# Kernel optimization log

Hardware: AMD Instinct MI355X
Metric: run time of the kernel (lower is better)

Reference implementation:

```python
import jax, jax.numpy as jnp
import numpy as np

RENDER_STEP = 0.005
N_FREQS = 6

def pos_enc(x):
    # x: [N,3] -> [N, 3 + 2*N_FREQS*3]
    freqs = (2.0 ** jnp.arange(N_FREQS, dtype=x.dtype)) * jnp.pi
    xb = x[:, None, :] * freqs[:, None]            # [N,F,3]
    enc = jnp.concatenate([jnp.sin(xb), jnp.cos(xb)], axis=-1).reshape(x.shape[0], -1)
    return jnp.concatenate([x, enc], axis=-1)

def geom_fwd(points, Wg0, bg0, Wg1, bg1, Wg2, bg2):
    h = jax.nn.relu(pos_enc(points) @ Wg0 + bg0)
    h = jax.nn.relu(h @ Wg1 + bg1)
    return h @ Wg2 + bg2                           # [N,16]; ch0 = sdf, full vec = features


def setup_inputs() -> dict:
    key = jax.random.key(0)
    ks = jax.random.split(key, 12)
    n_rays, n_samples = 16384, 524288
    sc = lambda fan_in: 1.0 / np.sqrt(fan_in)
    inp = {
        'rays_o': jax.random.normal(ks[0], (n_rays, 3), jnp.float32) * 0.5,
        'rays_d': jax.random.normal(ks[1], (n_rays, 3), jnp.float32),
        'ray_indices': jnp.sort(jax.random.randint(ks[2], (n_samples,), 0, n_rays, jnp.int32)),
        't_starts': jax.random.uniform(ks[3], (n_samples, 1), jnp.float32),
        'random_points': jax.random.normal(ks[4], (1024, 3), jnp.float32),
        's_var': jnp.ones((1,), jnp.float32),
        'Wg0': jax.random.normal(ks[5], (39, 256), jnp.float32) * sc(39),
        'bg0': jnp.zeros((256,), jnp.float32),
        'Wg1': jax.random.normal(ks[6], (256, 256), jnp.float32) * sc(256),
        'bg1': jnp.zeros((256,), jnp.float32),
        'Wg2': jax.random.normal(ks[7], (256, 16), jnp.float32) * sc(256),
        'bg2': jnp.zeros((16,), jnp.float32),
        'Wc0': jax.random.normal(ks[8], (25, 256), jnp.float32) * sc(25),
        'bc0': jnp.zeros((256,), jnp.float32),
        'Wc1': jax.random.normal(ks[9], (256, 3), jnp.float32) * sc(256),
        'bc1': jnp.zeros((3,), jnp.float32),
    }
    return inp


def reference(rays_o, rays_d, ray_indices, t_starts, random_points, s_var,
              Wg0, bg0, Wg1, bg1, Wg2, bg2, Wc0, bc0, Wc1, bc1):
    n_rays = rays_o.shape[0]
    rays_d = rays_d / (jnp.linalg.norm(rays_d, axis=-1, keepdims=True) + 1e-10)

    midpoints = t_starts + RENDER_STEP * 0.5       # [N,1]
    t_intervals = RENDER_STEP
    t_origins = rays_o[ray_indices]                # gather [N,3]
    t_dirs = rays_d[ray_indices]
    points = t_origins + t_dirs * midpoints        # [N,3]

    # SDF network forward + analytic gradient wrt points (one fwd + one bwd)
    out, vjp_fn = jax.vjp(lambda p: geom_fwd(p, Wg0, bg0, Wg1, bg1, Wg2, bg2), points)
    sdf = out[:, 0]                                # [N]
    feats = out                                    # [N,16]
    cot = jnp.zeros_like(out).at[:, 0].set(1.0)
    grad = vjp_fn(cot)[0]                          # dSDF/dpoints [N,3]
    normal = grad / (jnp.linalg.norm(grad, axis=-1, keepdims=True) + 1e-10)

    # color network: dirs + feats + points + normal -> rgb
    cin = jnp.concatenate([t_dirs, feats, points, normal], axis=-1)   # [N,25]
    rgbs = jax.nn.sigmoid(jax.nn.relu(cin @ Wc0 + bc0) @ Wc1 + bc1)   # [N,3]

    # get_alpha (cos_anneal_ratio = 1.0)
    inv_s = jnp.clip(jnp.exp(s_var[0]), 1e-6, 1e6)
    dSDF_dt = jnp.sum(grad * t_dirs, axis=-1, keepdims=True)
    dSDF_dt = -jax.nn.relu(-dSDF_dt)
    cdf = jax.nn.sigmoid(inv_s * sdf[:, None])
    rho = jnp.maximum(inv_s * (cdf - 1.0) * dSDF_dt, 0.0)
    alpha = 1.0 - jnp.exp(-rho * t_intervals)      # [N,1]

    # render_weight_from_alpha: per-ray exclusive cumprod of (1-alpha), log-space
    a = jnp.clip(alpha[:, 0], 0.0, 1.0 - 1e-7)
    loga = jnp.log1p(-a)
    E = jnp.cumsum(loga) - loga                    # exclusive cumsum
    starts = jnp.clip(jnp.searchsorted(ray_indices, jnp.arange(n_rays, dtype=ray_indices.dtype)),
                      0, a.shape[0] - 1)           # first sample idx per ray
    trans = jnp.exp(E - E[starts][ray_indices])    # per-ray transmittance
    weights = (a * trans)[:, None]                 # [N,1]

    seg = lambda v: jax.ops.segment_sum(weights * v, ray_indices, num_segments=n_rays)
    opacity = jax.ops.segment_sum(weights, ray_indices, num_segments=n_rays)  # [R,1]
    depth = seg(midpoints)
    pixels_color = seg(rgbs)
    pixels_normal = seg(normal)
    pixels_normal = pixels_normal / (jnp.linalg.norm(pixels_normal, axis=-1, keepdims=True) + 1e-10)

    random_sdfs = geom_fwd(random_points, Wg0, bg0, Wg1, bg1, Wg2, bg2)[:, :1]
    return (pixels_color, pixels_normal, opacity, depth, weights, sdf, random_sdfs)
```

## Files before the change

kernel.cpp:

```cpp
#include <hip/hip_runtime.h>
#include <math.h>


#define TILE 32
#define NTHREADS 512
#define LDP 264
#define LDE 72
#define LDCIN 40
#define PI_F 3.14159265358979323846f

typedef _Float16 half8 __attribute__((ext_vector_type(8)));
typedef float f32x4 __attribute__((ext_vector_type(4)));
typedef float f32x16 __attribute__((ext_vector_type(16)));

struct alignas(16) SMemK2 {
    _Float16 a0h[TILE * LDP];
    _Float16 a0l[TILE * LDP];
    _Float16 a1h[TILE * LDP];
    _Float16 a1l[TILE * LDP];
    _Float16 ench[TILE * LDE];
    _Float16 encl[TILE * LDE];
    float feats[TILE * 16];
    float pts [TILE * 4];
    float dirs[TILE * 4];
    float nrm [TILE * 4];
};

__device__ __forceinline__ void splitst(float v, _Float16* ph, _Float16* pl) {
    _Float16 h = (_Float16)v;
    *ph = h;
    *pl = (_Float16)(v - (float)h);
}

__device__ __forceinline__ f32x16 zero16() {
    f32x16 z;
#pragma unroll
    for (int i = 0; i < 16; ++i) z[i] = 0.f;
    return z;
}

template<int KITERS, bool BIAS, bool RELU, bool AMASK, bool CMASK, bool WLO>
__device__ __forceinline__ void gemm32(
    const _Float16* Ah, const _Float16* Al, const int lda,
    const _Float16* __restrict__ Bp, const float* __restrict__ bias,
    _Float16* Ch, _Float16* Cl, const int ldc,
    const int lane, const int nt)
{
    f32x16 acc0 = zero16(), acc1 = zero16();
    const int row  = lane & 31;
    const int koff = (lane >> 5) * 8;
    const _Float16* ahb = Ah + row * lda + koff;
    const _Float16* alb = Al + row * lda + koff;
    const _Float16* bbase = Bp + ((size_t)nt * KITERS * 64 + lane) * 16;

    half8 ax[2], ay[2];
    half8 bh[3], bl[3];
    ax[0] = *(const half8*)ahb;
    if (!AMASK) ay[0] = *(const half8*)alb;
    bh[0] = *(const half8*)bbase;
    if (!AMASK) bl[0] = *(const half8*)(bbase + 8);
    if (KITERS > 1) {
        bh[1] = *(const half8*)(bbase + 1024);
        if (!AMASK) bl[1] = *(const half8*)(bbase + 1024 + 8);
    }

#pragma unroll
    for (int kit = 0; kit < KITERS; ++kit) {
        const int ac = kit & 1, an = ac ^ 1;
        const int bc = kit % 3;
        if (kit + 1 < KITERS) {
            ax[an] = *(const half8*)(ahb + (kit + 1) * 16);
            if (!AMASK) ay[an] = *(const half8*)(alb + (kit + 1) * 16);
        }
        if (kit + 2 < KITERS) {
            const int bn = (kit + 2) % 3;
            const _Float16* bp = bbase + (size_t)(kit + 2) * 1024;
            bh[bn] = *(const half8*)bp;
            if (!AMASK) bl[bn] = *(const half8*)(bp + 8);
        }
        f32x16& acc = ac ? acc1 : acc0;
        if (AMASK) {
            half8 m;
#pragma unroll
            for (int j = 0; j < 8; ++j) {
                _Float16 t = ax[ac][j] * (_Float16)16384.f;
                m[j] = (t < (_Float16)1.f) ? t : (_Float16)1.f;
            }
            __builtin_amdgcn_s_setprio(1);
            acc = __builtin_amdgcn_mfma_f32_32x32x16_f16(m, bh[bc], acc, 0, 0, 0);
            __builtin_amdgcn_s_setprio(0);
        } else {
            __builtin_amdgcn_s_setprio(1);
            acc = __builtin_amdgcn_mfma_f32_32x32x16_f16(ay[ac], bh[bc], acc, 0, 0, 0);
            acc = __builtin_amdgcn_mfma_f32_32x32x16_f16(ax[ac], bl[bc], acc, 0, 0, 0);
            acc = __builtin_amdgcn_mfma_f32_32x32x16_f16(ax[ac], bh[bc], acc, 0, 0, 0);
            __builtin_amdgcn_s_setprio(0);
        }
    }
    const int col = lane & 31;
    const int rb  = (lane >> 5) * 4;
    const int jc  = nt * 32 + col;
    const float bs = BIAS ? bias[jc] : 0.f;
#pragma unroll
    for (int r = 0; r < 16; ++r) {
        const int srow = (r & 3) + 8 * (r >> 2) + rb;
        float v = acc0[r] + acc1[r] + bs;
        if (RELU) v = (v > 0.f) ? fmaxf(v, 1e-4f) : 0.f;
        if (CMASK) { if (!((float)Ch[srow * ldc + jc] > 0.f)) v = 0.f; }
        _Float16 h = (_Float16)v;
        Ch[srow * ldc + jc] = h;
        if (WLO) Cl[srow * ldc + jc] = (_Float16)(v - (float)h);
    }
}

template<int KITERS, int NTPW>
__device__ __forceinline__ void gemm16(
    const _Float16* Ah, const _Float16* Al, const int lda,
    const _Float16* __restrict__ Bp,
    _Float16* Ch, _Float16* Cl, const int ldc,
    const int lane, const int mt, const int ntbase)
{
    f32x4 acc[NTPW];
#pragma unroll
    for (int t = 0; t < NTPW; ++t) acc[t] = (f32x4){0.f, 0.f, 0.f, 0.f};
    const int m  = mt * 16 + (lane & 15);
    const int q8 = (lane >> 4) * 8;
    const _Float16* ahb = Ah + m * lda + q8;
    const _Float16* alb = Al + m * lda + q8;
    const _Float16* bbase = Bp + ((size_t)ntbase * KITERS * 64 + lane) * 16;

    half8 ax[2], ay[2], bh[3][NTPW], bl[3][NTPW];
    ax[0] = *(const half8*)ahb;
    ay[0] = *(const half8*)alb;
#pragma unroll
    for (int t = 0; t < NTPW; ++t) {
        const _Float16* bt = bbase + (size_t)t * KITERS * 1024;
        bh[0][t] = *(const half8*)bt;
        bl[0][t] = *(const half8*)(bt + 8);
    }
    if (KITERS > 1) {
#pragma unroll
        for (int t = 0; t < NTPW; ++t) {
            const _Float16* bt = bbase + 1024 + (size_t)t * KITERS * 1024;
            bh[1][t] = *(const half8*)bt;
            bl[1][t] = *(const half8*)(bt + 8);
        }
    }
#pragma unroll
    for (int kit = 0; kit < KITERS; ++kit) {
        const int ac = kit & 1, an = ac ^ 1;
        const int bc = kit % 3;
        if (kit + 1 < KITERS) {
            ax[an] = *(const half8*)(ahb + (kit + 1) * 32);
            ay[an] = *(const half8*)(alb + (kit + 1) * 32);
        }
        if (kit + 2 < KITERS) {
            const int bn = (kit + 2) % 3;
            const _Float16* bp = bbase + (size_t)(kit + 2) * 1024;
#pragma unroll
            for (int t = 0; t < NTPW; ++t) {
                const _Float16* bt = bp + (size_t)t * KITERS * 1024;
                bh[bn][t] = *(const half8*)bt;
                bl[bn][t] = *(const half8*)(bt + 8);
            }
        }
        __builtin_amdgcn_s_setprio(1);
#pragma unroll
        for (int t = 0; t < NTPW; ++t) {
            acc[t] = __builtin_amdgcn_mfma_f32_16x16x32_f16(ay[ac], bh[bc][t], acc[t], 0, 0, 0);
            acc[t] = __builtin_amdgcn_mfma_f32_16x16x32_f16(ax[ac], bl[bc][t], acc[t], 0, 0, 0);
            acc[t] = __builtin_amdgcn_mfma_f32_16x16x32_f16(ax[ac], bh[bc][t], acc[t], 0, 0, 0);
        }
        __builtin_amdgcn_s_setprio(0);
    }
    const int col = lane & 15, q = lane >> 4;
#pragma unroll
    for (int t = 0; t < NTPW; ++t) {
        const int j = (ntbase + t) * 16 + col;
#pragma unroll
        for (int r = 0; r < 4; ++r) {
            const int s = mt * 16 + q * 4 + r;
            float v = acc[t][r];
            _Float16 h = (_Float16)v;
            Ch[s * ldc + j] = h;
            Cl[s * ldc + j] = (_Float16)(v - (float)h);
        }
    }
}

__global__ __launch_bounds__(256) void k0_pack(
    const float* __restrict__ Wg0, const float* __restrict__ Wg1,
    const float* __restrict__ Wg2, const float* __restrict__ Wc0,
    const float* __restrict__ Wc1,
    _Float16* __restrict__ Wg0p, _Float16* __restrict__ Wg1p,
    _Float16* __restrict__ Wg1Tp, _Float16* __restrict__ Wg0Tp,
    _Float16* __restrict__ Wc0p, _Float16* __restrict__ Wg2p,
    _Float16* __restrict__ Wc1p)
{
    int gid = blockIdx.x * 256 + threadIdx.x;
    if (gid >= 176128) return;
    int idx, kiters, mode;
    _Float16* dst;
    if      (gid <  12288) { idx = gid;          kiters = 3;  dst = Wg0p;  mode = 0; }
    else if (gid <  77824) { idx = gid -  12288; kiters = 16; dst = Wg1p;  mode = 1; }
    else if (gid < 143360) { idx = gid -  77824; kiters = 16; dst = Wg1Tp; mode = 2; }
    else if (gid < 159744) { idx = gid - 143360; kiters = 8;  dst = Wg0Tp; mode = 3; }
    else if (gid < 167936) { idx = gid - 159744; kiters = 2;  dst = Wc0p;  mode = 4; }
    else if (gid < 172032) { idx = gid - 167936; kiters = 8;  dst = Wg2p;  mode = 5; }
    else                   { idx = gid - 172032; kiters = 8;  dst = Wc1p;  mode = 6; }
    const bool p32 = (mode == 0 || mode == 1 || mode == 2 || mode == 4);
    int j = idx & 7, lane = (idx >> 3) & 63, rest = idx >> 9;
    int kit = rest % kiters, nt = rest / kiters;
    int k, n;
    if (p32) { k = kit * 16 + ((lane >> 5) << 3) + j; n = (nt << 5) + (lane & 31); }
    else     { k = kit * 32 + ((lane >> 4) << 3) + j; n = (nt << 4) + (lane & 15); }
    float val = 0.f;
    switch (mode) {
        case 0: val = (k < 39) ? Wg0[k * 256 + n] : 0.f; break;
        case 1: val = Wg1[k * 256 + n]; break;
        case 2: val = Wg1[n * 256 + k] * Wg2[k * 16]; break;
        case 3: val = (n < 39) ? Wg0[n * 256 + k] : 0.f; break;
        case 4: val = (k < 25) ? Wc0[k * 256 + n] : 0.f; break;
        case 5: val = Wg2[k * 16 + n]; break;
        case 6: val = (n < 3) ? Wc1[k * 3 + n] : 0.f; break;
    }
    _Float16 h = (_Float16)val;
    _Float16 l = (_Float16)(val - (float)h);
    int off = ((nt * kiters + kit) * 64 + lane) * 16 + j;
    dst[off] = h;
    dst[off + 8] = l;
}

__global__ __launch_bounds__(512, 4) void k2_mlp(
    const float* __restrict__ rays_o, const float* __restrict__ rays_d,
    const int*   __restrict__ ray_idx, const float* __restrict__ t_starts,
    const float* __restrict__ s_var,
    const float* __restrict__ bg0, const float* __restrict__ bg1,
    const float* __restrict__ bg2,
    const float* __restrict__ bc0, const float* __restrict__ bc1,
    const _Float16* __restrict__ Wg0p, const _Float16* __restrict__ Wg1p,
    const _Float16* __restrict__ Wg1Tp, const _Float16* __restrict__ Wg0Tp,
    const _Float16* __restrict__ Wc0p, const _Float16* __restrict__ Wg2p,
    const _Float16* __restrict__ Wc1p,
    float* __restrict__ out_sdf, float* __restrict__ ws_a,
    float* __restrict__ ws_rgb, float* __restrict__ ws_nrm,
    int Nsamp)
{
    __shared__ SMemK2 sm;
    const int tid = threadIdx.x;
    const int lane = tid & 63;
    const int w = tid >> 6;
    const int n0 = blockIdx.x * TILE;

    if (tid < TILE) {
        int n = n0 + tid; if (n >= Nsamp) n = Nsamp - 1;
        int ri = ray_idx[n];
        float dx = rays_d[ri * 3 + 0], dy = rays_d[ri * 3 + 1], dz = rays_d[ri * 3 + 2];
        float inv = 1.f / (sqrtf(dx * dx + dy * dy + dz * dz) + 1e-10f);
        dx *= inv; dy *= inv; dz *= inv;
        float mid = t_starts[n] + 0.0025f;
        sm.dirs[tid * 4 + 0] = dx; sm.dirs[tid * 4 + 1] = dy; sm.dirs[tid * 4 + 2] = dz;
        float px = rays_o[ri * 3 + 0] + dx * mid;
        float py = rays_o[ri * 3 + 1] + dy * mid;
        float pz = rays_o[ri * 3 + 2] + dz * mid;
        sm.pts[tid * 4 + 0] = px; sm.pts[tid * 4 + 1] = py; sm.pts[tid * 4 + 2] = pz;
        splitst(px, &sm.ench[tid * LDE + 0], &sm.encl[tid * LDE + 0]);
        splitst(py, &sm.ench[tid * LDE + 1], &sm.encl[tid * LDE + 1]);
        splitst(pz, &sm.ench[tid * LDE + 2], &sm.encl[tid * LDE + 2]);
    }
    __syncthreads();

    for (int i = tid; i < TILE * 3; i += NTHREADS) {
        int s = i & 31;
        int d = i >> 5;
        float x = sm.pts[s * 4 + d];
        float a = PI_F * x;
        float sv = sinf(a), cv = cosf(a);
#pragma unroll
        for (int f = 0; f < 6; ++f) {
            splitst(sv, &sm.ench[s * LDE + 3 + f * 6 + d],     &sm.encl[s * LDE + 3 + f * 6 + d]);
            splitst(cv, &sm.ench[s * LDE + 3 + f * 6 + 3 + d], &sm.encl[s * LDE + 3 + f * 6 + 3 + d]);
            float s2 = 2.f * sv * cv;
            float c2 = 1.f - 2.f * sv * sv;
            sv = s2; cv = c2;
        }
    }
    for (int i = tid; i < TILE * 9; i += NTHREADS) {
        int s = i / 9, c = 39 + (i - s * 9);
        sm.ench[s * LDE + c] = (_Float16)0.f;
        sm.encl[s * LDE + c] = (_Float16)0.f;
    }
    __syncthreads();

    gemm32<3, true, true, false, false, true>(sm.ench, sm.encl, LDE,
                                              Wg0p, bg0, sm.a0h, sm.a0l, LDP, lane, w);
    __syncthreads();

    gemm32<16, true, true, false, false, true>(sm.a0h, sm.a0l, LDP,
                                               Wg1p, bg1, sm.a1h, sm.a1l, LDP, lane, w);
    __syncthreads();

    if (w < 2) {
        f32x4 acc = (f32x4){0.f, 0.f, 0.f, 0.f};
        const int m = w * 16 + (lane & 15);
        const int q8 = (lane >> 4) * 8;
        const _Float16* ahb = sm.a1h + m * LDP + q8;
        const _Float16* alb = sm.a1l + m * LDP + q8;
        const _Float16* bbase = Wg2p + lane * 16;
        half8 ax[2], ay[2], bh[2], bl[2];
        ax[0] = *(const half8*)ahb;
        ay[0] = *(const half8*)alb;
        bh[0] = *(const half8*)bbase;
        bl[0] = *(const half8*)(bbase + 8);
#pragma unroll
        for (int kit = 0; kit < 8; ++kit) {
            const int cur = kit & 1, nxt = cur ^ 1;
            if (kit + 1 < 8) {
                ax[nxt] = *(const half8*)(ahb + (kit + 1) * 32);
                ay[nxt] = *(const half8*)(alb + (kit + 1) * 32);
                const _Float16* bp = bbase + (kit + 1) * 1024;
                bh[nxt] = *(const half8*)bp;
                bl[nxt] = *(const half8*)(bp + 8);
            }
            __builtin_amdgcn_s_setprio(1);
            acc = __builtin_amdgcn_mfma_f32_16x16x32_f16(ay[cur], bh[cur], acc, 0, 0, 0);
            acc = __builtin_amdgcn_mfma_f32_16x16x32_f16(ax[cur], bl[cur], acc, 0, 0, 0);
            acc = __builtin_amdgcn_mfma_f32_16x16x32_f16(ax[cur], bh[cur], acc, 0, 0, 0);
            __builtin_amdgcn_s_setprio(0);
        }
        int col = lane & 15, q = lane >> 4;
        float bs = bg2[col];
#pragma unroll
        for (int r = 0; r < 4; ++r) {
            int s = w * 16 + q * 4 + r;
            float vv = acc[r] + bs;
            sm.feats[s * 16 + col] = vv;
            if (col == 0) { int n = n0 + s; if (n < Nsamp) out_sdf[n] = vv; }
        }
    }

    gemm32<16, false, false, true, true, true>(sm.a1h, sm.a1l, LDP,
                                               Wg1Tp, nullptr, sm.a0h, sm.a0l, LDP, lane, w);
    __syncthreads();

    gemm16<8, 1>(sm.a0h, sm.a0l, LDP, Wg0Tp,
                 sm.a1h, sm.a1l, LDP, lane, w & 1, w >> 1);
    __syncthreads();

    if (tid < TILE) {
        int s = tid;
        float g[3];
#pragma unroll
        for (int d = 0; d < 3; ++d)
            g[d] = (float)sm.a1h[s * LDP + d] + (float)sm.a1l[s * LDP + d];
#pragma unroll
        for (int f = 0; f < 6; ++f) {
            float freq = PI_F * (float)(1 << f);
#pragma unroll
            for (int d = 0; d < 3; ++d) {
                int cs = 3 + f * 6 + d, cc = cs + 3;
                float gs = (float)sm.a1h[s * LDP + cs] + (float)sm.a1l[s * LDP + cs];
                float gc = (float)sm.a1h[s * LDP + cc] + (float)sm.a1l[s * LDP + cc];
                float sv = (float)sm.ench[s * LDE + cs] + (float)sm.encl[s * LDE + cs];
                float cv = (float)sm.ench[s * LDE + cc] + (float)sm.encl[s * LDE + cc];
                g[d] += freq * (gs * cv - gc * sv);
            }
        }
        float gl = sqrtf(g[0] * g[0] + g[1] * g[1] + g[2] * g[2]);
        float invl = 1.f / (gl + 1e-10f);
        float nx = g[0] * invl, ny = g[1] * invl, nz = g[2] * invl;
        sm.nrm[s * 4 + 0] = nx; sm.nrm[s * 4 + 1] = ny; sm.nrm[s * 4 + 2] = nz;
        float dx = sm.dirs[s * 4 + 0], dy = sm.dirs[s * 4 + 1], dz = sm.dirs[s * 4 + 2];
        float dsdt = fminf(g[0] * dx + g[1] * dy + g[2] * dz, 0.f);
        float sdf = sm.feats[s * 16 + 0];
        float inv_s = __expf(s_var[0]);
        inv_s = fminf(fmaxf(inv_s, 1e-6f), 1e6f);
        float cdf = 1.f / (1.f + __expf(-inv_s * sdf));
        float rho = fmaxf(inv_s * (cdf - 1.f) * dsdt, 0.f);
        float alpha = 1.f - __expf(-rho * 0.005f);
        float a = fminf(fmaxf(alpha, 0.f), 1.f - 1e-7f);
        int n = n0 + s;
        if (n < Nsamp) {
            ws_a[n] = a;
            ws_nrm[n * 3 + 0] = nx; ws_nrm[n * 3 + 1] = ny; ws_nrm[n * 3 + 2] = nz;
        }
    }
    __syncthreads();

    _Float16* cinh = sm.a0h;
    _Float16* cinl = sm.a0l;
    for (int i = tid; i < TILE * 32; i += NTHREADS) {
        int s = i >> 5, c = i & 31;
        float v = 0.f;
        if      (c < 3)  v = sm.dirs[s * 4 + c];
        else if (c < 19) v = sm.feats[s * 16 + (c - 3)];
        else if (c < 22) v = sm.pts[s * 4 + (c - 19)];
        else if (c < 25) v = sm.nrm[s * 4 + (c - 22)];
        splitst(v, &cinh[s * LDCIN + c], &cinl[s * LDCIN + c]);
    }
    __syncthreads();

    gemm32<2, true, true, false, false, true>(cinh, cinl, LDCIN,
                                              Wc0p, bc0, sm.a1h, sm.a1l, LDP, lane, w);
    __syncthreads();

    if (w < 2) {
        f32x4 acc = (f32x4){0.f, 0.f, 0.f, 0.f};
        const int m = w * 16 + (lane & 15);
        const int q8 = (lane >> 4) * 8;
        const _Float16* ahb = sm.a1h + m * LDP + q8;
        const _Float16* alb = sm.a1l + m * LDP + q8;
        const _Float16* bbase = Wc1p + lane * 16;
        half8 ax[2], ay[2], bh[2], bl[2];
        ax[0] = *(const half8*)ahb;
        ay[0] = *(const half8*)alb;
        bh[0] = *(const half8*)bbase;
        bl[0] = *(const half8*)(bbase + 8);
#pragma unroll
        for (int kit = 0; kit < 8; ++kit) {
            const int cur = kit & 1, nxt = cur ^ 1;
            if (kit + 1 < 8) {
                ax[nxt] = *(const half8*)(ahb + (kit + 1) * 32);
                ay[nxt] = *(const half8*)(alb + (kit + 1) * 32);
                const _Float16* bp = bbase + (kit + 1) * 1024;
                bh[nxt] = *(const half8*)bp;
                bl[nxt] = *(const half8*)(bp + 8);
            }
            __builtin_amdgcn_s_setprio(1);
            acc = __builtin_amdgcn_mfma_f32_16x16x32_f16(ay[cur], bh[cur], acc, 0, 0, 0);
            acc = __builtin_amdgcn_mfma_f32_16x16x32_f16(ax[cur], bl[cur], acc, 0, 0, 0);
            acc = __builtin_amdgcn_mfma_f32_16x16x32_f16(ax[cur], bh[cur], acc, 0, 0, 0);
            __builtin_amdgcn_s_setprio(0);
        }
        int col = lane & 15, q = lane >> 4;
        if (col < 3) {
#pragma unroll
            for (int r = 0; r < 4; ++r) {
                int s = w * 16 + q * 4 + r;
                float rgb = 1.f / (1.f + __expf(-(acc[r] + bc1[col])));
                int n = n0 + s;
                if (n < Nsamp) ws_rgb[n * 3 + col] = rgb;
            }
        }
    }
}

__global__ void k3_composite(
    const int* __restrict__ ray_idx, const float* __restrict__ t_starts,
    const float* __restrict__ ws_a, const float* __restrict__ ws_rgb,
    const float* __restrict__ ws_nrm,
    float* __restrict__ out_pc, float* __restrict__ out_pn,
    float* __restrict__ out_op, float* __restrict__ out_dp,
    float* __restrict__ out_w, int n_rays, int Nsamp)
{
    int r = blockIdx.x * blockDim.x + threadIdx.x;
    if (r >= n_rays) return;
    int lo = 0, hi = Nsamp;
    while (lo < hi) { int m = (lo + hi) >> 1; if (ray_idx[m] < r) lo = m + 1; else hi = m; }
    int start = lo;
    hi = Nsamp;
    while (lo < hi) { int m = (lo + hi) >> 1; if (ray_idx[m] < r + 1) lo = m + 1; else hi = m; }
    int end = lo;

    float T = 1.f, aco = 0.f, acd = 0.f;
    float c0 = 0.f, c1 = 0.f, c2 = 0.f, nx = 0.f, ny = 0.f, nz = 0.f;
    for (int n = start; n < end; ++n) {
        float a = ws_a[n];
        float wgt = a * T;
        T *= (1.f - a);
        out_w[n] = wgt;
        float mid = t_starts[n] + 0.0025f;
        aco += wgt; acd += wgt * mid;
        c0 += wgt * ws_rgb[n * 3 + 0];
        c1 += wgt * ws_rgb[n * 3 + 1];
        c2 += wgt * ws_rgb[n * 3 + 2];
        nx += wgt * ws_nrm[n * 3 + 0];
        ny += wgt * ws_nrm[n * 3 + 1];
        nz += wgt * ws_nrm[n * 3 + 2];
    }
    out_op[r] = aco;
    out_dp[r] = acd;
    out_pc[r * 3 + 0] = c0; out_pc[r * 3 + 1] = c1; out_pc[r * 3 + 2] = c2;
    float nl = sqrtf(nx * nx + ny * ny + nz * nz);
    float inv = 1.f / (nl + 1e-10f);
    out_pn[r * 3 + 0] = nx * inv; out_pn[r * 3 + 1] = ny * inv; out_pn[r * 3 + 2] = nz * inv;
}

__global__ __launch_bounds__(256) void k4_random(
    const float* __restrict__ pts,
    const float* __restrict__ Wg0, const float* __restrict__ bg0,
    const float* __restrict__ Wg1, const float* __restrict__ bg1,
    const float* __restrict__ Wg2, const float* __restrict__ bg2,
    float* __restrict__ out_rs, int n_rand)
{
    __shared__ float enc[40];
    __shared__ float h[256];
    __shared__ float red[256];
    int b = blockIdx.x;
    if (b >= n_rand) return;
    int tid = threadIdx.x;
    if (tid < 39) {
        int c = tid;
        float v;
        if (c < 3) v = pts[b * 3 + c];
        else {
            int e = c - 3, f = e / 6, r = e - f * 6;
            float freq = PI_F * (float)(1 << f);
            int d = (r < 3) ? r : r - 3;
            float x = pts[b * 3 + d];
            v = (r < 3) ? sinf(freq * x) : cosf(freq * x);
        }
        enc[c] = v;
    }
    __syncthreads();
    {
        float z = bg0[tid];
        for (int m = 0; m < 39; ++m) z += enc[m] * Wg0[m * 256 + tid];
        h[tid] = fmaxf(z, 0.f);
    }
    __syncthreads();
    {
        float z = bg1[tid];
        for (int k = 0; k < 256; ++k) z += h[k] * Wg1[k * 256 + tid];
        float h1 = fmaxf(z, 0.f);
        red[tid] = h1 * Wg2[tid * 16];
    }
    __syncthreads();
    for (int off = 128; off > 0; off >>= 1) {
        if (tid < off) red[tid] += red[tid + off];
        __syncthreads();
    }
    if (tid == 0) out_rs[b] = red[0] + bg2[0];
}

extern "C" void kernel_launch(void* const* d_in, const int* in_sizes, int n_in,
                              void* d_out, int out_size, void* d_ws, size_t ws_size,
                              hipStream_t stream)
{
    const float* rays_o   = (const float*)d_in[0];
    const float* rays_d   = (const float*)d_in[1];
    const int*   ray_idx  = (const int*)  d_in[2];
    const float* t_starts = (const float*)d_in[3];
    const float* rpts     = (const float*)d_in[4];
    const float* s_var    = (const float*)d_in[5];
    const float* Wg0 = (const float*)d_in[6];  const float* bg0 = (const float*)d_in[7];
    const float* Wg1 = (const float*)d_in[8];  const float* bg1 = (const float*)d_in[9];
    const float* Wg2 = (const float*)d_in[10]; const float* bg2 = (const float*)d_in[11];
    const float* Wc0 = (const float*)d_in[12]; const float* bc0 = (const float*)d_in[13];
    const float* Wc1 = (const float*)d_in[14]; const float* bc1 = (const float*)d_in[15];

    const int n_rays = in_sizes[0] / 3;
    const int Ns     = in_sizes[2];
    const int n_rand = in_sizes[4] / 3;

    float* out  = (float*)d_out;
    float* o_pc = out;
    float* o_pn = out + (size_t)3 * n_rays;
    float* o_op = out + (size_t)6 * n_rays;
    float* o_dp = out + (size_t)7 * n_rays;
    float* o_w  = out + (size_t)8 * n_rays;
    float* o_sdf = o_w + Ns;
    float* o_rs  = o_sdf + Ns;

    _Float16* hptr  = (_Float16*)d_ws;
    _Float16* Wg0p  = hptr;
    _Float16* Wg1p  = Wg0p  + 24576;
    _Float16* Wg1Tp = Wg1p  + 131072;
    _Float16* Wg0Tp = Wg1Tp + 131072;
    _Float16* Wc0p  = Wg0Tp + 32768;
    _Float16* Wg2p  = Wc0p  + 16384;
    _Float16* Wc1p  = Wg2p  + 8192;
    float* fbase  = (float*)(hptr + 352256);
    float* ws_a   = fbase;
    float* ws_rgb = ws_a + Ns;
    float* ws_nrm = ws_rgb + (size_t)3 * Ns;

    hipLaunchKernelGGL(k0_pack, dim3(688), dim3(256), 0, stream,
                       Wg0, Wg1, Wg2, Wc0, Wc1,
                       Wg0p, Wg1p, Wg1Tp, Wg0Tp, Wc0p, Wg2p, Wc1p);
    hipLaunchKernelGGL(k2_mlp, dim3((Ns + TILE - 1) / TILE), dim3(NTHREADS), 0, stream,
                       rays_o, rays_d, ray_idx, t_starts, s_var,
                       bg0, bg1, bg2, bc0, bc1,
                       Wg0p, Wg1p, Wg1Tp, Wg0Tp, Wc0p, Wg2p, Wc1p,
                       o_sdf, ws_a, ws_rgb, ws_nrm, Ns);
    hipLaunchKernelGGL(k4_random, dim3(n_rand), dim3(256), 0, stream,
                       rpts, Wg0, bg0, Wg1, bg1, Wg2, bg2, o_rs, n_rand);
    hipLaunchKernelGGL(k3_composite, dim3((n_rays + 255) / 256), dim3(256), 0, stream,
                       ray_idx, t_starts, ws_a, ws_rgb, ws_nrm,
                       o_pc, o_pn, o_op, o_dp, o_w, n_rays, Ns);
}
```

Measured before the change: 712.2 us.

## Prefetch next-stage weight fragments across barriers and split narrow GEMMs over K

Before each __syncthreads, the first two B-fragments of the next GEMM stage are loaded into registers, so global weight latency overlaps the barrier wait. The two narrow 256x16 output GEMMs (geometry head and color head) previously ran on only 2 of 8 waves. They are now split across all 8 waves along K, and partial sums are combined with LDS atomicAdd into a bias-initialized buffer. The SDF output write moves into the later per-sample pass. The cost is higher register pressure from the held fragments plus LDS atomic contention, and float summation order now depends on atomic ordering.

```diff
diff --git a/kernel.cpp b/kernel.cpp
--- a/kernel.cpp
+++ b/kernel.cpp
@@ -26,6 +26,20 @@
     float nrm [TILE * 4];
 };
 
+struct BPre { half8 h0, l0, h1, l1; };
+
+template<bool LO>
+__device__ __forceinline__ BPre preB2(const _Float16* b) {
+    BPre p;
+    p.h0 = *(const half8*)b;
+    p.h1 = *(const half8*)(b + 1024);
+    if (LO) {
+        p.l0 = *(const half8*)(b + 8);
+        p.l1 = *(const half8*)(b + 1024 + 8);
+    }
+    return p;
+}
+
 __device__ __forceinline__ void splitst(float v, _Float16* ph, _Float16* pl) {
     _Float16 h = (_Float16)v;
     *ph = h;
@@ -42,7 +56,8 @@
 template<int KITERS, bool BIAS, bool RELU, bool AMASK, bool CMASK, bool WLO>
 __device__ __forceinline__ void gemm32(
     const _Float16* Ah, const _Float16* Al, const int lda,
-    const _Float16* __restrict__ Bp, const float* __restrict__ bias,
+    const _Float16* __restrict__ Bp, const BPre& pre,
+    const float* __restrict__ bias,
     _Float16* Ch, _Float16* Cl, const int ldc,
     const int lane, const int nt)
 {
@@ -55,14 +70,10 @@
 
     half8 ax[2], ay[2];
     half8 bh[3], bl[3];
+    bh[0] = pre.h0; bh[1] = pre.h1;
+    if (!AMASK) { bl[0] = pre.l0; bl[1] = pre.l1; }
     ax[0] = *(const half8*)ahb;
     if (!AMASK) ay[0] = *(const half8*)alb;
-    bh[0] = *(const half8*)bbase;
-    if (!AMASK) bl[0] = *(const half8*)(bbase + 8);
-    if (KITERS > 1) {
-        bh[1] = *(const half8*)(bbase + 1024);
-        if (!AMASK) bl[1] = *(const half8*)(bbase + 1024 + 8);
-    }
 
 #pragma unroll
     for (int kit = 0; kit < KITERS; ++kit) {
@@ -113,39 +124,25 @@
     }
 }
 
-template<int KITERS, int NTPW>
+template<int KITERS>
 __device__ __forceinline__ void gemm16(
     const _Float16* Ah, const _Float16* Al, const int lda,
-    const _Float16* __restrict__ Bp,
+    const _Float16* __restrict__ Bp, const BPre& pre,
     _Float16* Ch, _Float16* Cl, const int ldc,
     const int lane, const int mt, const int ntbase)
 {
-    f32x4 acc[NTPW];
-#pragma unroll
-    for (int t = 0; t < NTPW; ++t) acc[t] = (f32x4){0.f, 0.f, 0.f, 0.f};
+    f32x4 acc0 = (f32x4){0.f,0.f,0.f,0.f}, acc1 = (f32x4){0.f,0.f,0.f,0.f};
     const int m  = mt * 16 + (lane & 15);
     const int q8 = (lane >> 4) * 8;
     const _Float16* ahb = Ah + m * lda + q8;
     const _Float16* alb = Al + m * lda + q8;
     const _Float16* bbase = Bp + ((size_t)ntbase * KITERS * 64 + lane) * 16;
 
-    half8 ax[2], ay[2], bh[3][NTPW], bl[3][NTPW];
+    half8 ax[2], ay[2], bh[3], bl[3];
+    bh[0] = pre.h0; bl[0] = pre.l0;
+    bh[1] = pre.h1; bl[1] = pre.l1;
     ax[0] = *(const half8*)ahb;
     ay[0] = *(const half8*)alb;
-#pragma unroll
-    for (int t = 0; t < NTPW; ++t) {
-        const _Float16* bt = bbase + (size_t)t * KITERS * 1024;
-        bh[0][t] = *(const half8*)bt;
-        bl[0][t] = *(const half8*)(bt + 8);
-    }
-    if (KITERS > 1) {
-#pragma unroll
-        for (int t = 0; t < NTPW; ++t) {
-            const _Float16* bt = bbase + 1024 + (size_t)t * KITERS * 1024;
-            bh[1][t] = *(const half8*)bt;
-            bl[1][t] = *(const half8*)(bt + 8);
-        }
-    }
 #pragma unroll
     for (int kit = 0; kit < KITERS; ++kit) {
         const int ac = kit & 1, an = ac ^ 1;
@@ -157,35 +154,54 @@
         if (kit + 2 < KITERS) {
             const int bn = (kit + 2) % 3;
             const _Float16* bp = bbase + (size_t)(kit + 2) * 1024;
-#pragma unroll
-            for (int t = 0; t < NTPW; ++t) {
-                const _Float16* bt = bp + (size_t)t * KITERS * 1024;
-                bh[bn][t] = *(const half8*)bt;
-                bl[bn][t] = *(const half8*)(bt + 8);
-            }
-        }
+            bh[bn] = *(const half8*)bp;
+            bl[bn] = *(const half8*)(bp + 8);
+        }
+        f32x4& acc = ac ? acc1 : acc0;
         __builtin_amdgcn_s_setprio(1);
-#pragma unroll
-        for (int t = 0; t < NTPW; ++t) {
-            acc[t] = __builtin_amdgcn_mfma_f32_16x16x32_f16(ay[ac], bh[bc][t], acc[t], 0, 0, 0);
-            acc[t] = __builtin_amdgcn_mfma_f32_16x16x32_f16(ax[ac], bl[bc][t], acc[t], 0, 0, 0);
-            acc[t] = __builtin_amdgcn_mfma_f32_16x16x32_f16(ax[ac], bh[bc][t], acc[t], 0, 0, 0);
-        }
+        acc = __builtin_amdgcn_mfma_f32_16x16x32_f16(ay[ac], bh[bc], acc, 0, 0, 0);
+        acc = __builtin_amdgcn_mfma_f32_16x16x32_f16(ax[ac], bl[bc], acc, 0, 0, 0);
+        acc = __builtin_amdgcn_mfma_f32_16x16x32_f16(ax[ac], bh[bc], acc, 0, 0, 0);
         __builtin_amdgcn_s_setprio(0);
     }
     const int col = lane & 15, q = lane >> 4;
-#pragma unroll
-    for (int t = 0; t < NTPW; ++t) {
-        const int j = (ntbase + t) * 16 + col;
-#pragma unroll
-        for (int r = 0; r < 4; ++r) {
-            const int s = mt * 16 + q * 4 + r;
-            float v = acc[t][r];
-            _Float16 h = (_Float16)v;
-            Ch[s * ldc + j] = h;
-            Cl[s * ldc + j] = (_Float16)(v - (float)h);
-        }
-    }
+    const int j = ntbase * 16 + col;
+#pragma unroll
+    for (int r = 0; r < 4; ++r) {
+        const int s = mt * 16 + q * 4 + r;
+        float v = acc0[r] + acc1[r];
+        _Float16 h = (_Float16)v;
+        Ch[s * ldc + j] = h;
+        Cl[s * ldc + j] = (_Float16)(v - (float)h);
+    }
+}
+
+__device__ __forceinline__ void kpartial16(
+    const _Float16* Ah, const _Float16* Al,
+    const BPre& pre, float* red, const int lane, const int w)
+{
+    const int mt = w & 1, ks = w >> 1;
+    const int m  = mt * 16 + (lane & 15);
+    const int q8 = (lane >> 4) * 8;
+    const _Float16* ahb = Ah + m * LDP + q8 + ks * 64;
+    const _Float16* alb = Al + m * LDP + q8 + ks * 64;
+    half8 a0 = *(const half8*)ahb;
+    half8 y0 = *(const half8*)alb;
+    half8 a1 = *(const half8*)(ahb + 32);
+    half8 y1 = *(const half8*)(alb + 32);
+    f32x4 acc = (f32x4){0.f, 0.f, 0.f, 0.f};
+    __builtin_amdgcn_s_setprio(1);
+    acc = __builtin_amdgcn_mfma_f32_16x16x32_f16(y0, pre.h0, acc, 0, 0, 0);
+    acc = __builtin_amdgcn_mfma_f32_16x16x32_f16(a0, pre.l0, acc, 0, 0, 0);
+    acc = __builtin_amdgcn_mfma_f32_16x16x32_f16(a0, pre.h0, acc, 0, 0, 0);
+    acc = __builtin_amdgcn_mfma_f32_16x16x32_f16(y1, pre.h1, acc, 0, 0, 0);
+    acc = __builtin_amdgcn_mfma_f32_16x16x32_f16(a1, pre.l1, acc, 0, 0, 0);
+    acc = __builtin_amdgcn_mfma_f32_16x16x32_f16(a1, pre.h1, acc, 0, 0, 0);
+    __builtin_amdgcn_s_setprio(0);
+    const int col = lane & 15, q = lane >> 4;
+#pragma unroll
+    for (int r = 0; r < 4; ++r)
+        atomicAdd(&red[(mt * 16 + q * 4 + r) * 16 + col], acc[r]);
 }
 
 __global__ __launch_bounds__(256) void k0_pack(
@@ -252,6 +268,10 @@
     const int w = tid >> 6;
     const int n0 = blockIdx.x * TILE;
 
+    BPre preP2 = preB2<true>(Wg0p + ((size_t)w * 3 * 64 + lane) * 16);
+
+    for (int i = tid; i < TILE * 16; i += NTHREADS)
+        sm.feats[i] = bg2[i & 15];
     if (tid < TILE) {
         int n = n0 + tid; if (n >= Nsamp) n = Nsamp - 1;
         int ri = ray_idx[n];
@@ -293,58 +313,27 @@
     __syncthreads();
 
     gemm32<3, true, true, false, false, true>(sm.ench, sm.encl, LDE,
-                                              Wg0p, bg0, sm.a0h, sm.a0l, LDP, lane, w);
+                                              Wg0p, preP2, bg0, sm.a0h, sm.a0l, LDP, lane, w);
+    BPre preP3 = preB2<true>(Wg1p + ((size_t)w * 16 * 64 + lane) * 16);
     __syncthreads();
 
     gemm32<16, true, true, false, false, true>(sm.a0h, sm.a0l, LDP,
-                                               Wg1p, bg1, sm.a1h, sm.a1l, LDP, lane, w);
-    __syncthreads();
-
-    if (w < 2) {
-        f32x4 acc = (f32x4){0.f, 0.f, 0.f, 0.f};
-        const int m = w * 16 + (lane & 15);
-        const int q8 = (lane >> 4) * 8;
-        const _Float16* ahb = sm.a1h + m * LDP + q8;
-        const _Float16* alb = sm.a1l + m * LDP + q8;
-        const _Float16* bbase = Wg2p + lane * 16;
-        half8 ax[2], ay[2], bh[2], bl[2];
-        ax[0] = *(const half8*)ahb;
-        ay[0] = *(const half8*)alb;
-        bh[0] = *(const half8*)bbase;
-        bl[0] = *(const half8*)(bbase + 8);
-#pragma unroll
-        for (int kit = 0; kit < 8; ++kit) {
-            const int cur = kit & 1, nxt = cur ^ 1;
-            if (kit + 1 < 8) {
-                ax[nxt] = *(const half8*)(ahb + (kit + 1) * 32);
-                ay[nxt] = *(const half8*)(alb + (kit + 1) * 32);
-                const _Float16* bp = bbase + (kit + 1) * 1024;
-                bh[nxt] = *(const half8*)bp;
-                bl[nxt] = *(const half8*)(bp + 8);
-            }
-            __builtin_amdgcn_s_setprio(1);
-            acc = __builtin_amdgcn_mfma_f32_16x16x32_f16(ay[cur], bh[cur], acc, 0, 0, 0);
-            acc = __builtin_amdgcn_mfma_f32_16x16x32_f16(ax[cur], bl[cur], acc, 0, 0, 0);
-            acc = __builtin_amdgcn_mfma_f32_16x16x32_f16(ax[cur], bh[cur], acc, 0, 0, 0);
-            __builtin_amdgcn_s_setprio(0);
-        }
-        int col = lane & 15, q = lane >> 4;
-        float bs = bg2[col];
-#pragma unroll
-        for (int r = 0; r < 4; ++r) {
-            int s = w * 16 + q * 4 + r;
-            float vv = acc[r] + bs;
-            sm.feats[s * 16 + col] = vv;
-            if (col == 0) { int n = n0 + s; if (n < Nsamp) out_sdf[n] = vv; }
-        }
-    }
+                                               Wg1p, preP3, bg1, sm.a1h, sm.a1l, LDP, lane, w);
+    BPre preP6 = preB2<false>(Wg1Tp + ((size_t)w * 16 * 64 + lane) * 16);
+    BPre preP4 = preB2<true>(Wg2p + lane * 16 + (w >> 1) * 2048);
+    __syncthreads();
+
+    kpartial16(sm.a1h, sm.a1l, preP4, sm.feats, lane, w);
 
     gemm32<16, false, false, true, true, true>(sm.a1h, sm.a1l, LDP,
-                                               Wg1Tp, nullptr, sm.a0h, sm.a0l, LDP, lane, w);
-    __syncthreads();
-
-    gemm16<8, 1>(sm.a0h, sm.a0l, LDP, Wg0Tp,
-                 sm.a1h, sm.a1l, LDP, lane, w & 1, w >> 1);
+                                               Wg1Tp, preP6, nullptr, sm.a0h, sm.a0l, LDP, lane, w);
+    BPre preP7 = preB2<true>(Wg0Tp + ((size_t)(w >> 1) * 8 * 64 + lane) * 16);
+    __syncthreads();
+
+    if (w < 6)
+        gemm16<8>(sm.a0h, sm.a0l, LDP, Wg0Tp, preP7,
+                  sm.a1h, sm.a1l, LDP, lane, w & 1, w >> 1);
+    BPre preP8 = preB2<true>(Wc0p + ((size_t)w * 2 * 64 + lane) * 16);
     __syncthreads();
 
     if (tid < TILE) {
@@ -381,6 +370,7 @@
         float a = fminf(fmaxf(alpha, 0.f), 1.f - 1e-7f);
         int n = n0 + s;
         if (n < Nsamp) {
+            out_sdf[n] = sdf;
             ws_a[n] = a;
             ws_nrm[n * 3 + 0] = nx; ws_nrm[n * 3 + 1] = ny; ws_nrm[n * 3 + 2] = nz;
         }
@@ -400,46 +390,24 @@
     }
     __syncthreads();
 
+    for (int i = tid; i < TILE * 16; i += NTHREADS)
+        sm.feats[i] = ((i & 15) < 3) ? bc1[i & 15] : 0.f;
+
     gemm32<2, true, true, false, false, true>(cinh, cinl, LDCIN,
-                                              Wc0p, bc0, sm.a1h, sm.a1l, LDP, lane, w);
-    __syncthreads();
-
-    if (w < 2) {
-        f32x4 acc = (f32x4){0.f, 0.f, 0.f, 0.f};
-        const int m = w * 16 + (lane & 15);
-        const int q8 = (lane >> 4) * 8;
-        const _Float16* ahb = sm.a1h + m * LDP + q8;
-        const _Float16* alb = sm.a1l + m * LDP + q8;
-        const _Float16* bbase = Wc1p + lane * 16;
-        half8 ax[2], ay[2], bh[2], bl[2];
-        ax[0] = *(const half8*)ahb;
-        ay[0] = *(const half8*)alb;
-        bh[0] = *(const half8*)bbase;
-        bl[0] = *(const half8*)(bbase + 8);
-#pragma unroll
-        for (int kit = 0; kit < 8; ++kit) {
-            const int cur = kit & 1, nxt = cur ^ 1;
-            if (kit + 1 < 8) {
-                ax[nxt] = *(const half8*)(ahb + (kit + 1) * 32);
-                ay[nxt] = *(const half8*)(alb + (kit + 1) * 32);
-                const _Float16* bp = bbase + (kit + 1) * 1024;
-                bh[nxt] = *(const half8*)bp;
-                bl[nxt] = *(const half8*)(bp + 8);
-            }
-            __builtin_amdgcn_s_setprio(1);
-            acc = __builtin_amdgcn_mfma_f32_16x16x32_f16(ay[cur], bh[cur], acc, 0, 0, 0);
-            acc = __builtin_amdgcn_mfma_f32_16x16x32_f16(ax[cur], bl[cur], acc, 0, 0, 0);
-            acc = __builtin_amdgcn_mfma_f32_16x16x32_f16(ax[cur], bh[cur], acc, 0, 0, 0);
-            __builtin_amdgcn_s_setprio(0);
-        }
-        int col = lane & 15, q = lane >> 4;
-        if (col < 3) {
-#pragma unroll
-            for (int r = 0; r < 4; ++r) {
-                int s = w * 16 + q * 4 + r;
-                float rgb = 1.f / (1.f + __expf(-(acc[r] + bc1[col])));
-                int n = n0 + s;
-                if (n < Nsamp) ws_rgb[n * 3 + col] = rgb;
+                                              Wc0p, preP8, bc0, sm.a1h, sm.a1l, LDP, lane, w);
+    BPre preP9 = preB2<true>(Wc1p + lane * 16 + (w >> 1) * 2048);
+    __syncthreads();
+
+    kpartial16(sm.a1h, sm.a1l, preP9, sm.feats, lane, w);
+    __syncthreads();
+
+    if (tid < TILE) {
+        int n = n0 + tid;
+        if (n < Nsamp) {
+#pragma unroll
+            for (int c = 0; c < 3; ++c) {
+                float rgb = 1.f / (1.f + __expf(-sm.feats[tid * 16 + c]));
+                ws_rgb[n * 3 + c] = rgb;
             }
         }
     }
```

After: 951.6 us. 1.34x slower.
